# Kernel optimization log

Measured on AMD Instinct MI355X. Metric: run time of the kernel, lower is better.

The kernel has to match this reference:

```python
import jax, jax.numpy as jnp
import numpy as np

EPS = 1e-9
THRESHOLD = 0.2          # second_policy_eval = 'threshold'
CAP_FACTOR = 2.0         # capacity_factor_eval
MIN_EXPERT_CAPACITY = 4


def setup_inputs() -> dict:
    key = jax.random.key(0)
    k1, k2 = jax.random.split(key)
    x = jax.random.normal(k1, (8, 2048, 1024), dtype=jnp.float32)
    W = jax.random.normal(k2, (1024, 64), dtype=jnp.float32) * 0.02
    return {"x": x, "W": W}


def _cumsum_exclusive(t):
    # exclusive cumsum along token dim (-2)
    return jnp.cumsum(t, axis=-2) - t


def reference(x, W):
    b, n, d = x.shape
    e = W.shape[1]
    dt = x.dtype

    raw_gates = jax.nn.softmax(jnp.einsum('bnd,de->bne', x, W), axis=-1)  # [b,n,e]

    gate_1 = jnp.max(raw_gates, axis=-1)            # [b,n]
    index_1 = jnp.argmax(raw_gates, axis=-1)        # [b,n]
    mask_1 = jax.nn.one_hot(index_1, e, dtype=dt)   # [b,n,e]
    density_1_proxy = raw_gates

    gates_wo_top1 = raw_gates * (1.0 - mask_1)
    gate_2 = jnp.max(gates_wo_top1, axis=-1)
    index_2 = jnp.argmax(gates_wo_top1, axis=-1)
    mask_2 = jax.nn.one_hot(index_2, e, dtype=dt)

    denom = gate_1 + gate_2 + EPS
    gate_1 = gate_1 / denom
    gate_2 = gate_2 / denom

    density_1 = jnp.mean(mask_1, axis=-2)                         # [b,e]
    density_1_proxy_m = jnp.mean(density_1_proxy, axis=-2)        # [b,e]
    loss = jnp.mean(density_1_proxy_m * density_1) * float(e ** 2)

    # policy == 'threshold'
    mask_2 = mask_2 * (gate_2 > THRESHOLD).astype(dt)[..., None]

    expert_capacity = max(min(n, int(n * CAP_FACTOR / e)), MIN_EXPERT_CAPACITY)
    cap_f = float(expert_capacity)

    position_in_expert_1 = _cumsum_exclusive(mask_1) * mask_1
    mask_1 = mask_1 * (position_in_expert_1 < cap_f).astype(dt)
    mask_1_count = jnp.sum(mask_1, axis=-2, keepdims=True)        # [b,1,e]
    mask_1_flat = jnp.sum(mask_1, axis=-1)                        # [b,n]
    position_in_expert_1 = jnp.sum(position_in_expert_1, axis=-1) # [b,n]
    gate_1 = gate_1 * mask_1_flat

    position_in_expert_2 = _cumsum_exclusive(mask_2) + mask_1_count
    position_in_expert_2 = position_in_expert_2 * mask_2
    mask_2 = mask_2 * (position_in_expert_2 < cap_f).astype(dt)
    mask_2_flat = jnp.sum(mask_2, axis=-1)
    position_in_expert_2 = jnp.sum(position_in_expert_2, axis=-1)
    gate_2 = gate_2 * mask_2_flat

    # combine: [b, n, e, capacity]
    oh_e1 = jax.nn.one_hot(index_1, e, dtype=dt)[..., None]                                    # [b,n,e,1]
    oh_c1 = jax.nn.one_hot(position_in_expert_1.astype(jnp.int32), expert_capacity, dtype=dt)[..., None, :]  # [b,n,1,cap]
    oh_e2 = jax.nn.one_hot(index_2, e, dtype=dt)[..., None]
    oh_c2 = jax.nn.one_hot(position_in_expert_2.astype(jnp.int32), expert_capacity, dtype=dt)[..., None, :]

    combine_tensor = (
        (gate_1 * mask_1_flat)[..., None, None] * oh_e1 * oh_c1
        + (gate_2 * mask_2_flat)[..., None, None] * oh_e2 * oh_c2
    )
    dispatch_tensor = (combine_tensor != 0).astype(dt)
    return dispatch_tensor, combine_tensor, loss
```

## Files before the change

### kernel.cpp

```cpp
#include <hip/hip_runtime.h>
#include <math.h>

#define BB 8
#define NN 2048
#define DD 1024
#define EE 64
#define CAP 64
#define NTOK (BB * NN)
#define OUT_T_FLOATS 67108864
#define OUT_T_F4     16777216


__global__ __launch_bounds__(1024, 4) void gating_kernel(
    const float* __restrict__ x, const float* __restrict__ W,
    float4* __restrict__ recs, float* __restrict__ dens)
{
    __shared__ float xl[2][64][68];
    __shared__ float logits[64][65];
    __shared__ float dred[4][64];

    const int tid  = threadIdx.x;
    const int lane = tid & 63;
    const int wave = __builtin_amdgcn_readfirstlane(tid >> 6);
    const int tok0 = blockIdx.x * 64;

    const int srow = tid >> 4;
    const int scol = tid & 15;
    const float4* xsrc = (const float4*)(x + (size_t)(tok0 + srow) * DD) + scol;

    const float* wbase = W + wave * 4;

    float acc[4] = {0.f, 0.f, 0.f, 0.f};
    float4 pre = xsrc[0];

#pragma unroll 1
    for (int c = 0; c < 16; ++c) {
        *(float4*)&xl[c & 1][srow][scol * 4] = pre;
        if (c < 15) pre = xsrc[(c + 1) * 16];
        __syncthreads();
#pragma unroll
        for (int c4 = 0; c4 < 16; ++c4) {
            const float4 xv = *(const float4*)&xl[c & 1][lane][c4 * 4];
            const float xs[4] = {xv.x, xv.y, xv.z, xv.w};
#pragma unroll
            for (int kk = 0; kk < 4; ++kk) {
                const int k = c * 64 + c4 * 4 + kk;
                const float4 wv = *(const float4*)(wbase + (size_t)k * EE);
                acc[0] = fmaf(xs[kk], wv.x, acc[0]);
                acc[1] = fmaf(xs[kk], wv.y, acc[1]);
                acc[2] = fmaf(xs[kk], wv.z, acc[2]);
                acc[3] = fmaf(xs[kk], wv.w, acc[3]);
            }
        }
    }

#pragma unroll
    for (int j = 0; j < 4; ++j)
        logits[lane][wave * 4 + j] = acc[j];
    __syncthreads();

    if (wave < 4) {
        const int t0 = wave * 16;
        float densacc = 0.f;
#pragma unroll 1
        for (int ti = 0; ti < 16; ++ti) {
            const int t = t0 + ti;
            const float lv = logits[t][lane];

            float v = lv; int bi = lane;
#pragma unroll
            for (int off = 32; off; off >>= 1) {
                float ov = __shfl_xor(v, off);
                int   oi = __shfl_xor(bi, off);
                if (ov > v || (ov == v && oi < bi)) { v = ov; bi = oi; }
            }
            const float m1 = v; const int i1 = bi;
            float v2 = (lane == i1) ? -INFINITY : lv; int b2 = lane;
#pragma unroll
            for (int off = 32; off; off >>= 1) {
                float ov = __shfl_xor(v2, off);
                int   oi = __shfl_xor(b2, off);
                if (ov > v2 || (ov == v2 && oi < b2)) { v2 = ov; b2 = oi; }
            }
            const float m2 = v2; const int i2 = b2;

            float ex = expf(lv - m1);
            float Z = ex;
#pragma unroll
            for (int off = 32; off; off >>= 1) Z += __shfl_xor(Z, off);
            float g1 = 1.0f / Z;
            float g2 = expf(m2 - m1) * g1;
            float den = g1 + g2 + 1e-9f;
            float g1n = g1 / den;
            float g2n = g2 / den;
            int flag = (g2n > 0.2f) ? 1 : 0;

            densacc += ex * g1;

            if (lane == 0)
                recs[blockIdx.x * 64 + t] =
                    make_float4(g1n, g2n, __int_as_float(i1),
                                __int_as_float(i2 | (flag << 8)));
        }
        dred[wave][lane] = densacc;
    }
    __syncthreads();
    if (tid < 64) {
        float s = dred[0][tid] + dred[1][tid] + dred[2][tid] + dred[3][tid];
        dens[blockIdx.x * 64 + tid] = s;
    }
}

__global__ __launch_bounds__(1024) void scan_kernel(
    const float4* __restrict__ recs, const float* __restrict__ dens,
    float4* __restrict__ frecs, float* __restrict__ lossp)
{
    const int b = blockIdx.x;
    __shared__ int hist1[32][64], pre1[32][64];
    __shared__ int hist2[32][64], pre2[32][64];
    __shared__ int base2[64];
    __shared__ float dsum[64];

    const int tid = threadIdx.x;
    const int lane = tid & 63;
    const int wave = tid >> 6;

    float4 r[2];
    int e1[2], e2[2], fl[2], rank1[2], rank2[2];
    const unsigned long long below = (1ull << lane) - 1ull;

#pragma unroll
    for (int u = 0; u < 2; ++u) {
        const int g = 2 * wave + u;
        const int tok = g * 64 + lane;
        float4 rr = recs[b * NN + tok];
        r[u] = rr;
        e1[u] = __float_as_int(rr.z);
        int i2f = __float_as_int(rr.w);
        e2[u] = i2f & 63;
        fl[u] = i2f >> 8;

        unsigned long long m = ~0ull, mv = ~0ull;
#pragma unroll
        for (int bit = 0; bit < 6; ++bit) {
            unsigned long long vt = __ballot((e1[u] >> bit) & 1);
            m  &= ((e1[u] >> bit) & 1) ? vt : ~vt;
            mv &= ((lane  >> bit) & 1) ? vt : ~vt;
        }
        rank1[u] = __popcll(m & below);
        hist1[g][lane] = __popcll(mv);

        unsigned long long fv = __ballot(fl[u]);
        m = fv; mv = fv;
#pragma unroll
        for (int bit = 0; bit < 6; ++bit) {
            unsigned long long vt = __ballot((e2[u] >> bit) & 1);
            m  &= ((e2[u] >> bit) & 1) ? vt : ~vt;
            mv &= ((lane  >> bit) & 1) ? vt : ~vt;
        }
        rank2[u] = __popcll(m & below);
        hist2[g][lane] = __popcll(mv);
    }

    if (wave == 0) {
        float s = 0.f;
        for (int k = 0; k < 32; ++k) s += dens[(b * 32 + k) * 64 + lane];
        dsum[lane] = s;
    }
    __syncthreads();

    if (wave == 0) {
        int run = 0;
#pragma unroll
        for (int g = 0; g < 32; ++g) { pre1[g][lane] = run; run += hist1[g][lane]; }
        base2[lane] = run < CAP ? run : CAP;
        int run2 = 0;
#pragma unroll
        for (int g = 0; g < 32; ++g) { pre2[g][lane] = run2; run2 += hist2[g][lane]; }
        float v = dsum[lane] * (float)run;
#pragma unroll
        for (int off = 32; off; off >>= 1) v += __shfl_xor(v, off);
        if (lane == 0) lossp[b] = v;
    }
    __syncthreads();

#pragma unroll
    for (int u = 0; u < 2; ++u) {
        const int g = 2 * wave + u;
        const int tok = g * 64 + lane;
        int p1 = rank1[u] + pre1[g][e1[u]];
        int k1 = p1 < CAP;
        int p2 = rank2[u] + pre2[g][e2[u]] + base2[e2[u]];
        int k2 = fl[u] && (p2 < CAP);
        float4 fr;
        fr.x = k1 ? r[u].x : 0.f;
        fr.y = k2 ? r[u].y : 0.f;
        fr.z = __int_as_float(k1 ? (e1[u] * CAP + p1) : -1);
        fr.w = __int_as_float(k2 ? (e2[u] * CAP + p2) : -1);
        frecs[b * NN + tok] = fr;
    }
}

__global__ __launch_bounds__(256) void fill_kernel(
    const float4* __restrict__ frecs, const float* __restrict__ lossp,
    float* __restrict__ out)
{
    const int tid = blockIdx.x * 256 + threadIdx.x;
    const int token = tid >> 10;
    const int e  = (tid >> 4) & 63;
    const int c4 = tid & 15;
    float4 r = frecs[token];

    float cx = 0.f, cy = 0.f, cz = 0.f, cw = 0.f;
    float dx = 0.f, dy = 0.f, dz = 0.f, dw = 0.f;

    int p1 = __float_as_int(r.z);
    if (p1 >= 0 && (p1 >> 6) == e && ((p1 >> 2) & 15) == c4) {
        int cc = p1 & 3;
        if      (cc == 0) { cx = r.x; dx = 1.f; }
        else if (cc == 1) { cy = r.x; dy = 1.f; }
        else if (cc == 2) { cz = r.x; dz = 1.f; }
        else              { cw = r.x; dw = 1.f; }
    }
    int p2 = __float_as_int(r.w);
    if (p2 >= 0 && (p2 >> 6) == e && ((p2 >> 2) & 15) == c4) {
        int cc = p2 & 3;
        if      (cc == 0) { cx = r.y; dx = 1.f; }
        else if (cc == 1) { cy = r.y; dy = 1.f; }
        else if (cc == 2) { cz = r.y; dz = 1.f; }
        else              { cw = r.y; dw = 1.f; }
    }

    float4* o4 = (float4*)out;
    o4[tid]             = make_float4(dx, dy, dz, dw);
    o4[tid + OUT_T_F4]  = make_float4(cx, cy, cz, cw);

    if (tid == 0) {
        float s = 0.f;
        for (int k = 0; k < 8; ++k) s += lossp[k];
        out[2 * (size_t)OUT_T_FLOATS] = s * (1.0f / 524288.0f);
    }
}

extern "C" void kernel_launch(void* const* d_in, const int* in_sizes, int n_in,
                              void* d_out, int out_size, void* d_ws, size_t ws_size,
                              hipStream_t stream)
{
    const float* x = (const float*)d_in[0];
    const float* W = (const float*)d_in[1];
    float* out = (float*)d_out;
    char* ws = (char*)d_ws;

    float4* recs  = (float4*)(ws);
    float4* frecs = (float4*)(ws + 262144);
    float*  dens  = (float*)(ws + 524288);
    float*  lossp = (float*)(ws + 589824);

    gating_kernel<<<256, 1024, 0, stream>>>(x, W, recs, dens);
    scan_kernel<<<8, 1024, 0, stream>>>(recs, dens, frecs, lossp);
    fill_kernel<<<65536, 256, 0, stream>>>(frecs, lossp, out);
}
```

Baseline: 664.6 us.

## Register-tile gating GEMM with split-K across waves, direct global x loads

Rewrites the logits matmul in the gating kernel so each wave computes a 4-token by 8-expert register tile over half of the K dimension. x is read straight from global memory instead of through a double-buffered LDS stage with per-chunk barriers. Partial sums are reduced with lane shuffles and the two K halves are added when logits are read from LDS. This raises FMA reuse per loaded W value and removes 16 block barriers, at the cost of higher register pressure (32 accumulators) and possibly less coalesced x loads. The fill kernel, which likely dominates total time, is unchanged.

```diff
diff --git a/kernel.cpp b/kernel.cpp
--- a/kernel.cpp
+++ b/kernel.cpp
@@ -15,48 +15,75 @@
     const float* __restrict__ x, const float* __restrict__ W,
     float4* __restrict__ recs, float* __restrict__ dens)
 {
-    __shared__ float xl[2][64][68];
-    __shared__ float logits[64][65];
+    __shared__ float lg[2][64][68];
     __shared__ float dred[4][64];
 
     const int tid  = threadIdx.x;
     const int lane = tid & 63;
     const int wave = __builtin_amdgcn_readfirstlane(tid >> 6);
+    const int kh   = wave & 1;
+    const int eg   = wave >> 1;
+    const int r    = lane & 15;
+    const int q    = lane >> 4;
     const int tok0 = blockIdx.x * 64;
 
-    const int srow = tid >> 4;
-    const int scol = tid & 15;
-    const float4* xsrc = (const float4*)(x + (size_t)(tok0 + srow) * DD) + scol;
-
-    const float* wbase = W + wave * 4;
-
-    float acc[4] = {0.f, 0.f, 0.f, 0.f};
-    float4 pre = xsrc[0];
-
-#pragma unroll 1
-    for (int c = 0; c < 16; ++c) {
-        *(float4*)&xl[c & 1][srow][scol * 4] = pre;
-        if (c < 15) pre = xsrc[(c + 1) * 16];
-        __syncthreads();
-#pragma unroll
-        for (int c4 = 0; c4 < 16; ++c4) {
-            const float4 xv = *(const float4*)&xl[c & 1][lane][c4 * 4];
-            const float xs[4] = {xv.x, xv.y, xv.z, xv.w};
-#pragma unroll
-            for (int kk = 0; kk < 4; ++kk) {
-                const int k = c * 64 + c4 * 4 + kk;
-                const float4 wv = *(const float4*)(wbase + (size_t)k * EE);
-                acc[0] = fmaf(xs[kk], wv.x, acc[0]);
-                acc[1] = fmaf(xs[kk], wv.y, acc[1]);
-                acc[2] = fmaf(xs[kk], wv.z, acc[2]);
-                acc[3] = fmaf(xs[kk], wv.w, acc[3]);
+    float acc[4][8];
+#pragma unroll
+    for (int tt = 0; tt < 4; ++tt)
+#pragma unroll
+        for (int j = 0; j < 8; ++j) acc[tt][j] = 0.f;
+
+    const float4* xr[4];
+#pragma unroll
+    for (int tt = 0; tt < 4; ++tt)
+        xr[tt] = (const float4*)(x + (size_t)(tok0 + tt * 16 + r) * DD)
+                 + kh * 128 + q;
+    const float* wcol = W + eg * 8;
+
+#pragma unroll 2
+    for (int c = 0; c < 32; ++c) {
+        float4 xv[4];
+#pragma unroll
+        for (int tt = 0; tt < 4; ++tt) xv[tt] = xr[tt][c * 4];
+        const int k0 = (kh * 128 + c * 4 + q) * 4;
+#pragma unroll
+        for (int kk = 0; kk < 4; ++kk) {
+            const float* wrow = wcol + (size_t)(k0 + kk) * EE;
+            const float4 w0 = *(const float4*)(wrow);
+            const float4 w1 = *(const float4*)(wrow + 4);
+#pragma unroll
+            for (int tt = 0; tt < 4; ++tt) {
+                const float xs = ((const float*)&xv[tt])[kk];
+                acc[tt][0] = fmaf(xs, w0.x, acc[tt][0]);
+                acc[tt][1] = fmaf(xs, w0.y, acc[tt][1]);
+                acc[tt][2] = fmaf(xs, w0.z, acc[tt][2]);
+                acc[tt][3] = fmaf(xs, w0.w, acc[tt][3]);
+                acc[tt][4] = fmaf(xs, w1.x, acc[tt][4]);
+                acc[tt][5] = fmaf(xs, w1.y, acc[tt][5]);
+                acc[tt][6] = fmaf(xs, w1.z, acc[tt][6]);
+                acc[tt][7] = fmaf(xs, w1.w, acc[tt][7]);
             }
         }
     }
 
 #pragma unroll
-    for (int j = 0; j < 4; ++j)
-        logits[lane][wave * 4 + j] = acc[j];
+    for (int tt = 0; tt < 4; ++tt)
+#pragma unroll
+        for (int j = 0; j < 8; ++j) {
+            float v = acc[tt][j];
+            v += __shfl_xor(v, 16);
+            v += __shfl_xor(v, 32);
+            acc[tt][j] = v;
+        }
+    if (q == 0) {
+#pragma unroll
+        for (int tt = 0; tt < 4; ++tt) {
+            *(float4*)&lg[kh][tt * 16 + r][eg * 8]     =
+                make_float4(acc[tt][0], acc[tt][1], acc[tt][2], acc[tt][3]);
+            *(float4*)&lg[kh][tt * 16 + r][eg * 8 + 4] =
+                make_float4(acc[tt][4], acc[tt][5], acc[tt][6], acc[tt][7]);
+        }
+    }
     __syncthreads();
 
     if (wave < 4) {
@@ -65,7 +92,7 @@
 #pragma unroll 1
         for (int ti = 0; ti < 16; ++ti) {
             const int t = t0 + ti;
-            const float lv = logits[t][lane];
+            const float lv = lg[0][t][lane] + lg[1][t][lane];
 
             float v = lv; int bi = lane;
 #pragma unroll
```

After: 658.2 us. About the same (-1.0%).
